# Optimization experiments

Measured on AMD Instinct MI355X. Metric: run time of the kernel, lower is better.

## Reference

```python
import jax, jax.numpy as jnp
import numpy as np

GAMMA = 0.75
COST_DIA = 5.0
COST_DICE = 5.0
COST_CLS = 2.0
EPS = 1e-6


def setup_inputs() -> dict:
    key = jax.random.key(0)
    k1, k2, k3, k4 = jax.random.split(key, 4)
    B, T, N, L = 2, 4096, 128, 64
    preds_mask = jax.random.normal(k1, (B, T, N), jnp.float32)
    preds_class = jax.random.normal(k2, (B, N, 1), jnp.float32)
    targets = (jax.random.uniform(k3, (B, T, L)) < 0.3).astype(jnp.float32)
    weight = jnp.ones((N,), jnp.float32)           # buffer: weight_expanded
    alpha = jnp.full((N,), 0.3, jnp.float32)       # buffer: alpha_expanded
    beta = 1.0 - alpha                             # buffer: beta
    return {"preds_mask": preds_mask, "preds_class": preds_class,
            "targets": targets, "weight": weight, "alpha": alpha, "beta": beta}


def _batch_focal_loss(inputs, targets, weights, gamma, eps=EPS):
    # inputs: [N, T] logits; targets: [M, T] binary; weights: [M]
    N, T = inputs.shape
    pos = jax.nn.softplus(-inputs)  # BCE-with-logits vs 1
    neg = jax.nn.softplus(inputs)   # BCE-with-logits vs 0
    pos_bce = jnp.einsum('nt,mt->nmt', pos, targets)
    neg_bce = jnp.einsum('nt,mt->nmt', neg, 1.0 - targets)
    probs = jax.nn.sigmoid(inputs)[:, None, :]   # [N,1,T]
    t = targets[None, :, :]                      # [1,M,T]
    p_t = probs * t + (1.0 - probs) * (1.0 - t)
    focal_weight = (1.0 - p_t + eps) ** gamma
    bce_exp = pos_bce * t + neg_bce * (1.0 - t)
    focal = focal_weight * bce_exp               # [N,M,T]
    w = (weights / weights.sum())[None, :, None]
    return (w * focal).sum(axis=-1) / T          # [N,M]


def _batch_focal_tversky_loss(inputs, targets, weights, alpha, beta, gamma, eps=EPS):
    # inputs: [N, T] logits; targets: [M, T]
    p = jax.nn.sigmoid(inputs)
    tp = jnp.einsum('nt,mt->nm', p, targets)
    fp = jnp.einsum('nt,mt->nm', p, 1.0 - targets)
    fn = jnp.einsum('nt,mt->nm', 1.0 - p, targets)
    a = alpha[None, :]
    b = beta[None, :]
    w = weights / weights.sum()  # computed in torch code but unused in final expr
    tversky = (tp + eps) / (tp + a * fp + b * fn + eps)
    return (1.0 - tversky + eps) ** gamma        # [N,M]


def reference(preds_mask, preds_class, targets, weight, alpha, beta):
    # preds_mask: [B,T,N]; preds_class: [B,N,1]; targets: [B,T,L]
    L = targets.shape[-1]
    w = weight[:L]
    a = alpha[:L]
    bt = beta[:L]

    def per_batch(out_mask, cls, tgt):
        inp = out_mask.T   # [N,T]
        tg = tgt.T         # [L,T]
        cost_dia = _batch_focal_loss(inp, tg, w, 1.0 - GAMMA)
        cost_dice = _batch_focal_tversky_loss(inp, tg, w, a, bt, GAMMA)
        cost_cls = -jax.nn.sigmoid(cls)  # [N,1], broadcasts over L (== repeat(1,L))
        return COST_DIA * cost_dia + COST_DICE * cost_dice + COST_CLS * cost_cls

    # Full cost matrices C [B,N,L]. The scipy linear_sum_assignment step of the
    # original is a sequential CPU solve and is excluded from the GPU reference.
    return jax.vmap(per_batch)(preds_mask, preds_class, targets)
```

## Files before the change

### kernel.cpp

```cpp
#include <hip/hip_runtime.h>
#include <math.h>

#define B_ 2
#define T_ 4096
#define N_ 128
#define L_ 64
#define CT 64
#define NC (T_/CT)

constexpr float GAMMA_ = 0.75f;
constexpr float EPS_ = 1e-6f;

__global__ void __launch_bounds__(256)
k_fused(const float* __restrict__ preds, const float* __restrict__ targets,
        float* __restrict__ Cp_tp, float* __restrict__ Cp_dd,
        float* __restrict__ sumPp, float* __restrict__ sumBp,
        float* __restrict__ sumTp) {
    int bid = blockIdx.x;
    int b = bid >> 7;
    int c = (bid >> 1) & (NC - 1);
    int h = bid & 1;
    int tid = threadIdx.x;

    __shared__ float2 pd[64][CT + 1];
    __shared__ float  gs[64][CT + 1];
    __shared__ float  redA[4][64];
    __shared__ float  redB[4][64];
    __shared__ float  redT[4][64];

    int ln = tid & 63;
    int ti = tid >> 6;

    const float* pb = preds + ((size_t)b * T_ + (size_t)c * CT) * N_ + h * 64;
    float sp = 0.f, sb = 0.f;
#pragma unroll
    for (int i = 0; i < 16; ++i) {
        int t = 4 * i + ti;
        float x = pb[t * N_ + ln];
        float e = expf(-x);
        float p = 1.f / (1.f + e);
        float spn = log1pf(e);
        float spp = x + spn;
        float A  = sqrtf(sqrtf(1.f - p + EPS_)) * spn;
        float Bv = sqrtf(sqrtf(p + EPS_)) * spp;
        pd[ln][t] = make_float2(p, A - Bv);
        sp += p;
        sb += Bv;
    }
    redA[ti][ln] = sp;
    redB[ti][ln] = sb;

    const float* tb = targets + ((size_t)b * T_ + (size_t)c * CT) * L_;
    float st = 0.f;
#pragma unroll
    for (int i = 0; i < 16; ++i) {
        int t = 4 * i + ti;
        float v = tb[t * L_ + ln];
        gs[ln][t] = v;
        st += v;
    }
    redT[ti][ln] = st;
    __syncthreads();

    if (tid < 64) {
        float s1 = redA[0][tid] + redA[1][tid] + redA[2][tid] + redA[3][tid];
        float s2 = redB[0][tid] + redB[1][tid] + redB[2][tid] + redB[3][tid];
        size_t o = ((size_t)b * N_ + h * 64 + tid) * NC + c;
        sumPp[o] = s1;
        sumBp[o] = s2;
    } else if (h == 0 && tid < 128) {
        int mm = tid - 64;
        float s = redT[0][mm] + redT[1][mm] + redT[2][mm] + redT[3][mm];
        sumTp[((size_t)b * L_ + mm) * NC + c] = s;
    }

    int in = tid >> 4;
    int jm = tid & 15;
    float atp[4][4] = {{0.f}};
    float add_[4][4] = {{0.f}};
#pragma unroll 4
    for (int t = 0; t < CT; ++t) {
        float2 pv[4];
#pragma unroll
        for (int r = 0; r < 4; ++r) pv[r] = pd[in * 4 + r][t];
        float gv[4];
#pragma unroll
        for (int s = 0; s < 4; ++s) gv[s] = gs[jm + 16 * s][t];
#pragma unroll
        for (int r = 0; r < 4; ++r)
#pragma unroll
            for (int s = 0; s < 4; ++s) {
                atp[r][s]  = fmaf(pv[r].x, gv[s], atp[r][s]);
                add_[r][s] = fmaf(pv[r].y, gv[s], add_[r][s]);
            }
    }

#pragma unroll
    for (int r = 0; r < 4; ++r) {
        int n = h * 64 + in * 4 + r;
        size_t base = (((size_t)b * N_ + n) * NC + c) * L_;
#pragma unroll
        for (int s = 0; s < 4; ++s) {
            int m = jm + 16 * s;
            Cp_tp[base + m] = atp[r][s];
            Cp_dd[base + m] = add_[r][s];
        }
    }
}

__global__ void __launch_bounds__(256)
k_final(const float* __restrict__ preds_class, const float* __restrict__ weight,
        const float* __restrict__ alpha, const float* __restrict__ beta,
        const float* __restrict__ Cp_tp, const float* __restrict__ Cp_dd,
        const float* __restrict__ sumPp, const float* __restrict__ sumBp,
        const float* __restrict__ sumTp, float* __restrict__ out) {
    int bid = blockIdx.x;
    int b = bid >> 7;
    int n = bid & 127;
    int tid = threadIdx.x;
    int q = tid >> 6;
    int m = tid & 63;

    __shared__ float rtp[4][64];
    __shared__ float rdd[4][64];
    __shared__ float rst[4][64];
    __shared__ float ssp, ssb;

    size_t cbase = (((size_t)b * N_ + n) * NC) * L_ + m;
    float tp = 0.f, dd = 0.f;
#pragma unroll
    for (int k = 0; k < 16; ++k) {
        size_t o = cbase + (size_t)(q * 16 + k) * L_;
        tp += Cp_tp[o];
        dd += Cp_dd[o];
    }
    rtp[q][m] = tp;
    rdd[q][m] = dd;

    const float* stp_ = sumTp + ((size_t)b * L_ + m) * NC + q * 16;
    float st = 0.f;
#pragma unroll
    for (int k = 0; k < 16; ++k) st += stp_[k];
    rst[q][m] = st;

    if (tid < 64) {
        float v = sumPp[((size_t)b * N_ + n) * NC + tid];
        for (int o = 32; o > 0; o >>= 1) v += __shfl_xor(v, o);
        if (tid == 0) ssp = v;
    } else if (tid < 128) {
        int l = tid - 64;
        float v = sumBp[((size_t)b * N_ + n) * NC + l];
        for (int o = 32; o > 0; o >>= 1) v += __shfl_xor(v, o);
        if (l == 0) ssb = v;
    }
    __syncthreads();

    if (q == 0) {
        float tpt = rtp[0][m] + rtp[1][m] + rtp[2][m] + rtp[3][m];
        float ddt = rdd[0][m] + rdd[1][m] + rdd[2][m] + rdd[3][m];
        float stt = rst[0][m] + rst[1][m] + rst[2][m] + rst[3][m];
        float sp = ssp, sb = ssb;

        float wv = weight[m];
        float ws = wv;
        for (int o = 32; o > 0; o >>= 1) ws += __shfl_xor(ws, o);

        float a  = alpha[m];
        float bb = beta[m];

        float cost_dia = (wv / ws) * (sb + ddt) * (1.0f / (float)T_);

        float fpv = sp - tpt;
        float fnv = stt - tpt;
        float tv = (tpt + EPS_) / (tpt + a * fpv + bb * fnv + EPS_);
        float cost_dice = powf(1.f - tv + EPS_, GAMMA_);

        float cls = preds_class[b * N_ + n];
        float sig = 1.f / (1.f + expf(-cls));

        out[((size_t)b * N_ + n) * L_ + m] = 5.f * cost_dia + 5.f * cost_dice - 2.f * sig;
    }
}

extern "C" void kernel_launch(void* const* d_in, const int* in_sizes, int n_in,
                              void* d_out, int out_size, void* d_ws, size_t ws_size,
                              hipStream_t stream) {
    const float* preds_mask  = (const float*)d_in[0];
    const float* preds_class = (const float*)d_in[1];
    const float* targets     = (const float*)d_in[2];
    const float* weight      = (const float*)d_in[3];
    const float* alpha       = (const float*)d_in[4];
    const float* beta        = (const float*)d_in[5];
    float* out = (float*)d_out;

    float* Cp_tp = (float*)d_ws;
    float* Cp_dd = Cp_tp + (size_t)B_ * N_ * NC * L_;
    float* sumPp = Cp_dd + (size_t)B_ * N_ * NC * L_;
    float* sumBp = sumPp + (size_t)B_ * N_ * NC;
    float* sumTp = sumBp + (size_t)B_ * N_ * NC;

    k_fused<<<B_ * NC * 2, 256, 0, stream>>>(preds_mask, targets,
                                             Cp_tp, Cp_dd, sumPp, sumBp, sumTp);
    k_final<<<B_ * N_, 256, 0, stream>>>(preds_class, weight, alpha, beta,
                                         Cp_tp, Cp_dd, sumPp, sumBp, sumTp, out);
}
```

Baseline: 83.32 us.

## Vectorize loads/stores with float4 and transpose targets smem and partial layout

The first kernel now loads preds and targets as float4 and splits the float2 prob/diff shared array into two separate arrays. Targets are stored time-major so each inner-loop step reads a float4 of targets. Partial results are written as float4 in a chunk-major layout, and the final kernel's indexing is updated to match. The aim is fewer memory instructions and fewer LDS transactions, at the cost of larger reduction buffers and a different access pattern in the final reduction.

```diff
diff --git a/kernel.cpp b/kernel.cpp
--- a/kernel.cpp
+++ b/kernel.cpp
@@ -22,55 +22,70 @@
     int h = bid & 1;
     int tid = threadIdx.x;
 
-    __shared__ float2 pd[64][CT + 1];
-    __shared__ float  gs[64][CT + 1];
-    __shared__ float  redA[4][64];
-    __shared__ float  redB[4][64];
-    __shared__ float  redT[4][64];
-
-    int ln = tid & 63;
-    int ti = tid >> 6;
+    __shared__ float pdx[64][CT + 1];
+    __shared__ float pdy[64][CT + 1];
+    __shared__ float gs[CT][68];
+    __shared__ float redA[16][65];
+    __shared__ float redB[16][65];
+    __shared__ float redT[16][65];
+
+    int q4 = tid & 15;
+    int tq = tid >> 4;
 
     const float* pb = preds + ((size_t)b * T_ + (size_t)c * CT) * N_ + h * 64;
-    float sp = 0.f, sb = 0.f;
-#pragma unroll
-    for (int i = 0; i < 16; ++i) {
-        int t = 4 * i + ti;
-        float x = pb[t * N_ + ln];
-        float e = expf(-x);
-        float p = 1.f / (1.f + e);
-        float spn = log1pf(e);
-        float spp = x + spn;
-        float A  = sqrtf(sqrtf(1.f - p + EPS_)) * spn;
-        float Bv = sqrtf(sqrtf(p + EPS_)) * spp;
-        pd[ln][t] = make_float2(p, A - Bv);
-        sp += p;
-        sb += Bv;
-    }
-    redA[ti][ln] = sp;
-    redB[ti][ln] = sb;
+    float sA[4] = {0.f, 0.f, 0.f, 0.f};
+    float sB[4] = {0.f, 0.f, 0.f, 0.f};
+#pragma unroll
+    for (int i = 0; i < 4; ++i) {
+        int t = tq + 16 * i;
+        float4 x4 = *(const float4*)&pb[(size_t)t * N_ + 4 * q4];
+        float xs[4] = {x4.x, x4.y, x4.z, x4.w};
+#pragma unroll
+        for (int j = 0; j < 4; ++j) {
+            float x = xs[j];
+            float e = expf(-x);
+            float p = 1.f / (1.f + e);
+            float spn = log1pf(e);
+            float spp = x + spn;
+            float A  = sqrtf(sqrtf(1.f - p + EPS_)) * spn;
+            float Bv = sqrtf(sqrtf(p + EPS_)) * spp;
+            pdx[4 * q4 + j][t] = p;
+            pdy[4 * q4 + j][t] = A - Bv;
+            sA[j] += p;
+            sB[j] += Bv;
+        }
+    }
+#pragma unroll
+    for (int j = 0; j < 4; ++j) {
+        redA[tq][4 * q4 + j] = sA[j];
+        redB[tq][4 * q4 + j] = sB[j];
+    }
 
     const float* tb = targets + ((size_t)b * T_ + (size_t)c * CT) * L_;
-    float st = 0.f;
-#pragma unroll
-    for (int i = 0; i < 16; ++i) {
-        int t = 4 * i + ti;
-        float v = tb[t * L_ + ln];
-        gs[ln][t] = v;
-        st += v;
-    }
-    redT[ti][ln] = st;
+    float sT[4] = {0.f, 0.f, 0.f, 0.f};
+#pragma unroll
+    for (int i = 0; i < 4; ++i) {
+        int t = tq + 16 * i;
+        float4 g4 = *(const float4*)&tb[(size_t)t * L_ + 4 * q4];
+        *(float4*)&gs[t][4 * q4] = g4;
+        sT[0] += g4.x; sT[1] += g4.y; sT[2] += g4.z; sT[3] += g4.w;
+    }
+#pragma unroll
+    for (int j = 0; j < 4; ++j) redT[tq][4 * q4 + j] = sT[j];
     __syncthreads();
 
     if (tid < 64) {
-        float s1 = redA[0][tid] + redA[1][tid] + redA[2][tid] + redA[3][tid];
-        float s2 = redB[0][tid] + redB[1][tid] + redB[2][tid] + redB[3][tid];
+        float s1 = 0.f, s2 = 0.f;
+#pragma unroll
+        for (int k = 0; k < 16; ++k) { s1 += redA[k][tid]; s2 += redB[k][tid]; }
         size_t o = ((size_t)b * N_ + h * 64 + tid) * NC + c;
         sumPp[o] = s1;
         sumBp[o] = s2;
     } else if (h == 0 && tid < 128) {
         int mm = tid - 64;
-        float s = redT[0][mm] + redT[1][mm] + redT[2][mm] + redT[3][mm];
+        float s = 0.f;
+#pragma unroll
+        for (int k = 0; k < 16; ++k) s += redT[k][mm];
         sumTp[((size_t)b * L_ + mm) * NC + c] = s;
     }
 
@@ -78,33 +93,31 @@
     int jm = tid & 15;
     float atp[4][4] = {{0.f}};
     float add_[4][4] = {{0.f}};
-#pragma unroll 4
+#pragma unroll 2
     for (int t = 0; t < CT; ++t) {
-        float2 pv[4];
-#pragma unroll
-        for (int r = 0; r < 4; ++r) pv[r] = pd[in * 4 + r][t];
-        float gv[4];
-#pragma unroll
-        for (int s = 0; s < 4; ++s) gv[s] = gs[jm + 16 * s][t];
+        float4 gv = *(float4*)&gs[t][4 * jm];
+        float gvs[4] = {gv.x, gv.y, gv.z, gv.w};
+        float px[4], py[4];
+#pragma unroll
+        for (int r = 0; r < 4; ++r) {
+            px[r] = pdx[in * 4 + r][t];
+            py[r] = pdy[in * 4 + r][t];
+        }
 #pragma unroll
         for (int r = 0; r < 4; ++r)
 #pragma unroll
             for (int s = 0; s < 4; ++s) {
-                atp[r][s]  = fmaf(pv[r].x, gv[s], atp[r][s]);
-                add_[r][s] = fmaf(pv[r].y, gv[s], add_[r][s]);
+                atp[r][s]  = fmaf(px[r], gvs[s], atp[r][s]);
+                add_[r][s] = fmaf(py[r], gvs[s], add_[r][s]);
             }
     }
 
 #pragma unroll
     for (int r = 0; r < 4; ++r) {
         int n = h * 64 + in * 4 + r;
-        size_t base = (((size_t)b * N_ + n) * NC + c) * L_;
-#pragma unroll
-        for (int s = 0; s < 4; ++s) {
-            int m = jm + 16 * s;
-            Cp_tp[base + m] = atp[r][s];
-            Cp_dd[base + m] = add_[r][s];
-        }
+        size_t base = (((size_t)(b * NC + c)) * N_ + n) * L_ + 4 * jm;
+        *(float4*)&Cp_tp[base] = make_float4(atp[r][0], atp[r][1], atp[r][2], atp[r][3]);
+        *(float4*)&Cp_dd[base] = make_float4(add_[r][0], add_[r][1], add_[r][2], add_[r][3]);
     }
 }
 
@@ -126,11 +139,10 @@
     __shared__ float rst[4][64];
     __shared__ float ssp, ssb;
 
-    size_t cbase = (((size_t)b * N_ + n) * NC) * L_ + m;
     float tp = 0.f, dd = 0.f;
 #pragma unroll
     for (int k = 0; k < 16; ++k) {
-        size_t o = cbase + (size_t)(q * 16 + k) * L_;
+        size_t o = (((size_t)(b * NC + q * 16 + k)) * N_ + n) * L_ + m;
         tp += Cp_tp[o];
         dd += Cp_dd[o];
     }
```

New measurement: 84.25 us. Within noise of the previous version (+1.1%).
